# Optimization experiments

Measured on AMD Instinct MI355X. Metric: run time of the kernel, lower is better.

## Reference

```python
import jax, jax.numpy as jnp
import numpy as np

D_K = 64
SCALE = 1.0 / np.sqrt(D_K).astype(np.float32)
NEG_INF = -1e9


def setup_inputs() -> dict:
    key = jax.random.key(0)
    kq, kk, kv, km = jax.random.split(key, 4)
    B, H, S, D = 2, 16, 2048, D_K
    Q = jax.random.normal(kq, (B, H, S, D), dtype=jnp.float32)
    K = jax.random.normal(kk, (B, H, S, D), dtype=jnp.float32)
    V = jax.random.normal(kv, (B, H, S, D), dtype=jnp.float32)
    atten_mask = jax.random.randint(km, (B, H, S, S), 0, 2, dtype=jnp.int32)
    return {"Q": Q, "K": K, "V": V, "atten_mask": atten_mask}


def reference(Q, K, V, atten_mask):
    # scores: [B, H, Sq, Sk]
    scores = jnp.einsum("bhqd,bhkd->bhqk", Q, K) * SCALE
    scores = jnp.where(atten_mask.astype(bool), NEG_INF, scores)
    weights = jax.nn.softmax(scores, axis=-1)
    context = jnp.einsum("bhqk,bhkd->bhqd", weights, V)
    return (context, weights)
```

## Files before the change

kernel.cpp:

```cpp
#include <hip/hip_runtime.h>


#define S_LEN 2048
#define D_HEAD 64
#define BM 32
#define BN 64
#define NKB (S_LEN / BN)
#define CTX_ELEMS (2 * 16 * 2048 * 64)

typedef __attribute__((ext_vector_type(4))) float f32x4;
typedef __attribute__((ext_vector_type(8))) __bf16 bf16x8;
typedef __attribute__((ext_vector_type(2))) __bf16 bf16x2;

__device__ __forceinline__ bf16x8 pack8(f32x4 a, f32x4 b, float sc) {
    bf16x8 r;
    r[0] = (__bf16)(a[0] * sc); r[1] = (__bf16)(a[1] * sc);
    r[2] = (__bf16)(a[2] * sc); r[3] = (__bf16)(a[3] * sc);
    r[4] = (__bf16)(b[0] * sc); r[5] = (__bf16)(b[1] * sc);
    r[6] = (__bf16)(b[2] * sc); r[7] = (__bf16)(b[3] * sc);
    return r;
}


__global__ __launch_bounds__(256) void attn_fwd(
    const float* __restrict__ Qg, const float* __restrict__ Kg,
    const float* __restrict__ Vg, const int* __restrict__ Mg,
    float* __restrict__ outg)
{
    __shared__ __align__(16) __bf16 Vt[2][64][72];
    __shared__ __align__(16) __bf16 Pb[2][32][72];
    __shared__ unsigned short bmap[32][128];
    __shared__ float redl[4][32];
    __shared__ float invl[32];

    const int tid  = threadIdx.x;
    const int wave = tid >> 6;
    const int lane = tid & 63;
    const int c    = lane & 15;
    const int quad = lane >> 4;

    const int bid  = blockIdx.x;
    const int bh   = bid >> 6;
    const int row0 = (bid & 63) * BM;

    const float* Qh = Qg + (size_t)bh * S_LEN * D_HEAD;
    const float* Kh = Kg + (size_t)bh * S_LEN * D_HEAD;
    const float* Vh = Vg + (size_t)bh * S_LEN * D_HEAD;
    const int*   Mh = Mg + ((size_t)bh * S_LEN + row0) * S_LEN;
    float* ctx  = outg + ((size_t)bh * S_LEN + row0) * D_HEAD;
    float* wout = outg + (size_t)CTX_ELEMS + ((size_t)bh * S_LEN + row0) * S_LEN;

    bf16x8 aQ[2][2];
    #pragma unroll
    for (int t = 0; t < 2; ++t)
      #pragma unroll
      for (int h = 0; h < 2; ++h) {
        const float* p = Qh + (size_t)(row0 + 16 * t + c) * D_HEAD + 32 * h + quad * 8;
        aQ[t][h] = pack8(*(const f32x4*)p, *(const f32x4*)(p + 4), 0.125f);
      }

    f32x4 accO[2];
    accO[0] = (f32x4){0.f, 0.f, 0.f, 0.f};
    accO[1] = (f32x4){0.f, 0.f, 0.f, 0.f};
    float lacc[2][4] = {{0.f,0.f,0.f,0.f},{0.f,0.f,0.f,0.f}};

    const int vk2 = (tid & 31) * 2;
    const int vd8 = (tid >> 5) * 8;

    int buf = 0;
    for (int kb = 0; kb < NKB; ++kb) {
        const int k0 = kb * BN;

        {
            const float* vp = Vh + (size_t)(k0 + vk2) * D_HEAD + vd8;
            f32x4 r0a = *(const f32x4*)vp;
            f32x4 r0b = *(const f32x4*)(vp + 4);
            f32x4 r1a = *(const f32x4*)(vp + D_HEAD);
            f32x4 r1b = *(const f32x4*)(vp + D_HEAD + 4);
            #pragma unroll
            for (int i = 0; i < 4; ++i) {
                bf16x2 p0; p0[0] = (__bf16)r0a[i]; p0[1] = (__bf16)r1a[i];
                *(bf16x2*)&Vt[buf][vd8 + i][vk2] = p0;
                bf16x2 p1; p1[0] = (__bf16)r0b[i]; p1[1] = (__bf16)r1b[i];
                *(bf16x2*)&Vt[buf][vd8 + 4 + i][vk2] = p1;
            }
        }

        bf16x8 bK[2];
        #pragma unroll
        for (int h = 0; h < 2; ++h) {
            const float* p = Kh + (size_t)(k0 + 16 * wave + c) * D_HEAD + 32 * h + quad * 8;
            bK[h] = pack8(*(const f32x4*)p, *(const f32x4*)(p + 4), 1.0f);
        }
        f32x4 scv[2];
        scv[0] = (f32x4){0.f,0.f,0.f,0.f};
        scv[1] = (f32x4){0.f,0.f,0.f,0.f};
        #pragma unroll
        for (int h = 0; h < 2; ++h) {
            scv[0] = __builtin_amdgcn_mfma_f32_16x16x32_bf16(aQ[0][h], bK[h], scv[0], 0, 0, 0);
            scv[1] = __builtin_amdgcn_mfma_f32_16x16x32_bf16(aQ[1][h], bK[h], scv[1], 0, 0, 0);
        }

        #pragma unroll
        for (int t = 0; t < 2; ++t)
          #pragma unroll
          for (int r = 0; r < 4; ++r) {
            const int lrow = 16 * t + 4 * quad + r;
            const int col  = k0 + 16 * wave + c;
            const int mv   = __builtin_nontemporal_load(Mh + (size_t)lrow * S_LEN + col);
            const unsigned long long bal = __ballot(mv != 0);
            const float pv = mv ? 0.f : __expf(scv[t][r]);
            lacc[t][r] += pv;
            Pb[buf][lrow][16 * wave + c] = (__bf16)pv;
            if (c == 0)
                bmap[lrow][4 * kb + wave] = (unsigned short)(bal >> (16 * quad));
          }
        __syncthreads();

        #pragma unroll
        for (int h = 0; h < 2; ++h) {
            bf16x8 bV  = *(const bf16x8*)&Vt[buf][16 * wave + c][32 * h + quad * 8];
            bf16x8 aP0 = *(const bf16x8*)&Pb[buf][c][32 * h + quad * 8];
            bf16x8 aP1 = *(const bf16x8*)&Pb[buf][16 + c][32 * h + quad * 8];
            accO[0] = __builtin_amdgcn_mfma_f32_16x16x32_bf16(aP0, bV, accO[0], 0, 0, 0);
            accO[1] = __builtin_amdgcn_mfma_f32_16x16x32_bf16(aP1, bV, accO[1], 0, 0, 0);
        }
        buf ^= 1;
    }

    #pragma unroll
    for (int t = 0; t < 2; ++t)
      #pragma unroll
      for (int r = 0; r < 4; ++r) {
        float v = lacc[t][r];
        v += __shfl_xor(v, 1);
        v += __shfl_xor(v, 2);
        v += __shfl_xor(v, 4);
        v += __shfl_xor(v, 8);
        lacc[t][r] = v;
      }
    if (c == 0) {
        #pragma unroll
        for (int t = 0; t < 2; ++t)
          #pragma unroll
          for (int r = 0; r < 4; ++r)
            redl[wave][16 * t + 4 * quad + r] = lacc[t][r];
    }
    __syncthreads();
    if (tid < 32) {
        float s = redl[0][tid] + redl[1][tid] + redl[2][tid] + redl[3][tid];
        invl[tid] = 1.0f / s;
    }
    __syncthreads();

    float inv[2][4];
    #pragma unroll
    for (int t = 0; t < 2; ++t)
      #pragma unroll
      for (int r = 0; r < 4; ++r)
        inv[t][r] = invl[16 * t + 4 * quad + r];

    #pragma unroll
    for (int t = 0; t < 2; ++t)
      #pragma unroll
      for (int r = 0; r < 4; ++r)
        ctx[(size_t)(16 * t + 4 * quad + r) * D_HEAD + 16 * wave + c] = accO[t][r] * inv[t][r];

    for (int kb = 0; kb < NKB; ++kb) {
        const int k0 = kb * BN;
        bf16x8 bK[2];
        #pragma unroll
        for (int h = 0; h < 2; ++h) {
            const float* p = Kh + (size_t)(k0 + 16 * wave + c) * D_HEAD + 32 * h + quad * 8;
            bK[h] = pack8(*(const f32x4*)p, *(const f32x4*)(p + 4), 1.0f);
        }
        f32x4 scv[2];
        scv[0] = (f32x4){0.f,0.f,0.f,0.f};
        scv[1] = (f32x4){0.f,0.f,0.f,0.f};
        #pragma unroll
        for (int h = 0; h < 2; ++h) {
            scv[0] = __builtin_amdgcn_mfma_f32_16x16x32_bf16(aQ[0][h], bK[h], scv[0], 0, 0, 0);
            scv[1] = __builtin_amdgcn_mfma_f32_16x16x32_bf16(aQ[1][h], bK[h], scv[1], 0, 0, 0);
        }
        #pragma unroll
        for (int t = 0; t < 2; ++t)
          #pragma unroll
          for (int r = 0; r < 4; ++r) {
            const int lrow = 16 * t + 4 * quad + r;
            const unsigned bits = bmap[lrow][4 * kb + wave];
            const float pv = ((bits >> c) & 1u) ? 0.f : __expf(scv[t][r]) * inv[t][r];
            __builtin_nontemporal_store(pv, wout + (size_t)lrow * S_LEN + k0 + 16 * wave + c);
          }
    }
}

extern "C" void kernel_launch(void* const* d_in, const int* in_sizes, int n_in,
                              void* d_out, int out_size, void* d_ws, size_t ws_size,
                              hipStream_t stream) {
    const float* Q = (const float*)d_in[0];
    const float* K = (const float*)d_in[1];
    const float* V = (const float*)d_in[2];
    const int*   M = (const int*)d_in[3];
    float* out = (float*)d_out;
    dim3 grid(2048);
    dim3 block(256);
    attn_fwd<<<grid, block, 0, stream>>>(Q, K, V, M, out);
}
```

Baseline: 1.383 ms.

## Software-prefetch next K/V/mask tiles into registers in both attention passes

```diff
diff --git a/kernel.cpp b/kernel.cpp
--- a/kernel.cpp
+++ b/kernel.cpp
@@ -17,12 +17,24 @@
     r[0] = (__bf16)(a[0] * sc); r[1] = (__bf16)(a[1] * sc);
     r[2] = (__bf16)(a[2] * sc); r[3] = (__bf16)(a[3] * sc);
     r[4] = (__bf16)(b[0] * sc); r[5] = (__bf16)(b[1] * sc);
+    r[6] = (__bf16)(b[2] * sc); r[7] = (__bf16)(b[7 - 7] * sc);
     r[6] = (__bf16)(b[2] * sc); r[7] = (__bf16)(b[3] * sc);
     return r;
 }
 
-
-__global__ __launch_bounds__(256) void attn_fwd(
+#define MFMA16(a, b, c) __builtin_amdgcn_mfma_f32_16x16x32_bf16(a, b, c, 0, 0, 0)
+
+struct PF1 {
+    f32x4 v[4];
+    f32x4 k[4];
+    int   m[8];
+};
+struct PF2 {
+    f32x4 k[4];
+};
+
+
+__global__ __launch_bounds__(256, 4) void attn_fwd(
     const float* __restrict__ Qg, const float* __restrict__ Kg,
     const float* __restrict__ Vg, const int* __restrict__ Mg,
     float* __restrict__ outg)
@@ -67,65 +79,90 @@
     const int vk2 = (tid & 31) * 2;
     const int vd8 = (tid >> 5) * 8;
 
+#define ISSUE_V(P, KN) {                                                      \
+    const float* vp_ = Vh + (size_t)((KN) * BN + vk2) * D_HEAD + vd8;         \
+    (P).v[0] = *(const f32x4*)vp_;                                            \
+    (P).v[1] = *(const f32x4*)(vp_ + 4);                                      \
+    (P).v[2] = *(const f32x4*)(vp_ + D_HEAD);                                 \
+    (P).v[3] = *(const f32x4*)(vp_ + D_HEAD + 4); }
+
+#define ISSUE_K(P, KN) {                                                      \
+    const float* kp_ = Kh + (size_t)((KN) * BN + 16 * wave + c) * D_HEAD + quad * 8; \
+    (P).k[0] = *(const f32x4*)kp_;                                            \
+    (P).k[1] = *(const f32x4*)(kp_ + 4);                                      \
+    (P).k[2] = *(const f32x4*)(kp_ + 32);                                     \
+    (P).k[3] = *(const f32x4*)(kp_ + 36); }
+
+#define ISSUE_M(P, KN) {                                                      \
+    const int* mp_ = Mh + (KN) * BN + 16 * wave + c;                          \
+    _Pragma("unroll")                                                         \
+    for (int t_ = 0; t_ < 2; ++t_)                                            \
+      _Pragma("unroll")                                                       \
+      for (int r_ = 0; r_ < 4; ++r_)                                          \
+        (P).m[4 * t_ + r_] =                                                  \
+            __builtin_nontemporal_load(mp_ + (size_t)(16 * t_ + 4 * quad + r_) * S_LEN); }
+
+#define LDS_BARRIER() {                                                       \
+    asm volatile("s_waitcnt lgkmcnt(0)" ::: "memory");                        \
+    __builtin_amdgcn_s_barrier(); }
+
+#define P1BODY(KB, CUR, NXT) {                                                \
+    const int kn_ = ((KB) + 1 < NKB) ? (KB) + 1 : (KB);                       \
+        \
+    _Pragma("unroll")                                                         \
+    for (int i_ = 0; i_ < 4; ++i_) {                                          \
+        bf16x2 p0_; p0_[0] = (__bf16)CUR.v[0][i_]; p0_[1] = (__bf16)CUR.v[2][i_]; \
+        *(bf16x2*)&Vt[buf][vd8 + i_][vk2] = p0_;                              \
+        bf16x2 p1_; p1_[0] = (__bf16)CUR.v[1][i_]; p1_[1] = (__bf16)CUR.v[3][i_]; \
+        *(bf16x2*)&Vt[buf][vd8 + 4 + i_][vk2] = p1_;                          \
+    }                                                                         \
+    ISSUE_V(NXT, kn_);                                                        \
+                     \
+    bf16x8 bK0_ = pack8(CUR.k[0], CUR.k[1], 1.0f);                            \
+    bf16x8 bK1_ = pack8(CUR.k[2], CUR.k[3], 1.0f);                            \
+    ISSUE_K(NXT, kn_);                                                        \
+    f32x4 sc0_ = (f32x4){0.f, 0.f, 0.f, 0.f};                                 \
+    f32x4 sc1_ = (f32x4){0.f, 0.f, 0.f, 0.f};                                 \
+    sc0_ = MFMA16(aQ[0][0], bK0_, sc0_);                                      \
+    sc1_ = MFMA16(aQ[1][0], bK0_, sc1_);                                      \
+    sc0_ = MFMA16(aQ[0][1], bK1_, sc0_);                                      \
+    sc1_ = MFMA16(aQ[1][1], bK1_, sc1_);                                      \
+     \
+    _Pragma("unroll")                                                         \
+    for (int t_ = 0; t_ < 2; ++t_)                                            \
+      _Pragma("unroll")                                                       \
+      for (int r_ = 0; r_ < 4; ++r_) {                                        \
+        const int lrow_ = 16 * t_ + 4 * quad + r_;                            \
+        const int mv_   = CUR.m[4 * t_ + r_];                                 \
+        const unsigned long long bal_ = __ballot(mv_ != 0);                   \
+        const float sv_ = (t_ == 0) ? sc0_[r_] : sc1_[r_];                    \
+        const float pv_ = mv_ ? 0.f : __expf(sv_);                            \
+        lacc[t_][r_] += pv_;                                                  \
+        Pb[buf][lrow_][16 * wave + c] = (__bf16)pv_;                          \
+        if (c == 0)                                                           \
+            bmap[lrow_][4 * (KB) + wave] = (unsigned short)(bal_ >> (16 * quad)); \
+      }                                                                       \
+    ISSUE_M(NXT, kn_);                                                        \
+    LDS_BARRIER();                                                            \
+            \
+    _Pragma("unroll")                                                         \
+    for (int h_ = 0; h_ < 2; ++h_) {                                          \
+        bf16x8 bV_  = *(const bf16x8*)&Vt[buf][16 * wave + c][32 * h_ + quad * 8]; \
+        bf16x8 aP0_ = *(const bf16x8*)&Pb[buf][c][32 * h_ + quad * 8];        \
+        bf16x8 aP1_ = *(const bf16x8*)&Pb[buf][16 + c][32 * h_ + quad * 8];   \
+        accO[0] = MFMA16(aP0_, bV_, accO[0]);                                 \
+        accO[1] = MFMA16(aP1_, bV_, accO[1]);                                 \
+    }                                                                         \
+    buf ^= 1; }
+
     int buf = 0;
-    for (int kb = 0; kb < NKB; ++kb) {
-        const int k0 = kb * BN;
-
-        {
-            const float* vp = Vh + (size_t)(k0 + vk2) * D_HEAD + vd8;
-            f32x4 r0a = *(const f32x4*)vp;
-            f32x4 r0b = *(const f32x4*)(vp + 4);
-            f32x4 r1a = *(const f32x4*)(vp + D_HEAD);
-            f32x4 r1b = *(const f32x4*)(vp + D_HEAD + 4);
-            #pragma unroll
-            for (int i = 0; i < 4; ++i) {
-                bf16x2 p0; p0[0] = (__bf16)r0a[i]; p0[1] = (__bf16)r1a[i];
-                *(bf16x2*)&Vt[buf][vd8 + i][vk2] = p0;
-                bf16x2 p1; p1[0] = (__bf16)r0b[i]; p1[1] = (__bf16)r1b[i];
-                *(bf16x2*)&Vt[buf][vd8 + 4 + i][vk2] = p1;
-            }
-        }
-
-        bf16x8 bK[2];
-        #pragma unroll
-        for (int h = 0; h < 2; ++h) {
-            const float* p = Kh + (size_t)(k0 + 16 * wave + c) * D_HEAD + 32 * h + quad * 8;
-            bK[h] = pack8(*(const f32x4*)p, *(const f32x4*)(p + 4), 1.0f);
-        }
-        f32x4 scv[2];
-        scv[0] = (f32x4){0.f,0.f,0.f,0.f};
-        scv[1] = (f32x4){0.f,0.f,0.f,0.f};
-        #pragma unroll
-        for (int h = 0; h < 2; ++h) {
-            scv[0] = __builtin_amdgcn_mfma_f32_16x16x32_bf16(aQ[0][h], bK[h], scv[0], 0, 0, 0);
-            scv[1] = __builtin_amdgcn_mfma_f32_16x16x32_bf16(aQ[1][h], bK[h], scv[1], 0, 0, 0);
-        }
-
-        #pragma unroll
-        for (int t = 0; t < 2; ++t)
-          #pragma unroll
-          for (int r = 0; r < 4; ++r) {
-            const int lrow = 16 * t + 4 * quad + r;
-            const int col  = k0 + 16 * wave + c;
-            const int mv   = __builtin_nontemporal_load(Mh + (size_t)lrow * S_LEN + col);
-            const unsigned long long bal = __ballot(mv != 0);
-            const float pv = mv ? 0.f : __expf(scv[t][r]);
-            lacc[t][r] += pv;
-            Pb[buf][lrow][16 * wave + c] = (__bf16)pv;
-            if (c == 0)
-                bmap[lrow][4 * kb + wave] = (unsigned short)(bal >> (16 * quad));
-          }
-        __syncthreads();
-
-        #pragma unroll
-        for (int h = 0; h < 2; ++h) {
-            bf16x8 bV  = *(const bf16x8*)&Vt[buf][16 * wave + c][32 * h + quad * 8];
-            bf16x8 aP0 = *(const bf16x8*)&Pb[buf][c][32 * h + quad * 8];
-            bf16x8 aP1 = *(const bf16x8*)&Pb[buf][16 + c][32 * h + quad * 8];
-            accO[0] = __builtin_amdgcn_mfma_f32_16x16x32_bf16(aP0, bV, accO[0], 0, 0, 0);
-            accO[1] = __builtin_amdgcn_mfma_f32_16x16x32_bf16(aP1, bV, accO[1], 0, 0, 0);
-        }
-        buf ^= 1;
+    PF1 pf0, pf1;
+    ISSUE_V(pf0, 0);
+    ISSUE_K(pf0, 0);
+    ISSUE_M(pf0, 0);
+    for (int kb = 0; kb < NKB; kb += 2) {
+        P1BODY(kb,     pf0, pf1);
+        P1BODY(kb + 1, pf1, pf0);
     }
 
     #pragma unroll
@@ -166,31 +203,34 @@
       for (int r = 0; r < 4; ++r)
         ctx[(size_t)(16 * t + 4 * quad + r) * D_HEAD + 16 * wave + c] = accO[t][r] * inv[t][r];
 
-    for (int kb = 0; kb < NKB; ++kb) {
-        const int k0 = kb * BN;
-        bf16x8 bK[2];
-        #pragma unroll
-        for (int h = 0; h < 2; ++h) {
-            const float* p = Kh + (size_t)(k0 + 16 * wave + c) * D_HEAD + 32 * h + quad * 8;
-            bK[h] = pack8(*(const f32x4*)p, *(const f32x4*)(p + 4), 1.0f);
-        }
-        f32x4 scv[2];
-        scv[0] = (f32x4){0.f,0.f,0.f,0.f};
-        scv[1] = (f32x4){0.f,0.f,0.f,0.f};
-        #pragma unroll
-        for (int h = 0; h < 2; ++h) {
-            scv[0] = __builtin_amdgcn_mfma_f32_16x16x32_bf16(aQ[0][h], bK[h], scv[0], 0, 0, 0);
-            scv[1] = __builtin_amdgcn_mfma_f32_16x16x32_bf16(aQ[1][h], bK[h], scv[1], 0, 0, 0);
-        }
-        #pragma unroll
-        for (int t = 0; t < 2; ++t)
-          #pragma unroll
-          for (int r = 0; r < 4; ++r) {
-            const int lrow = 16 * t + 4 * quad + r;
-            const unsigned bits = bmap[lrow][4 * kb + wave];
-            const float pv = ((bits >> c) & 1u) ? 0.f : __expf(scv[t][r]) * inv[t][r];
-            __builtin_nontemporal_store(pv, wout + (size_t)lrow * S_LEN + k0 + 16 * wave + c);
-          }
+#define P2BODY(KB, CUR, NXT) {                                                \
+    const int kn_ = ((KB) + 1 < NKB) ? (KB) + 1 : (KB);                       \
+    ISSUE_K(NXT, kn_);                                                        \
+    bf16x8 bK0_ = pack8(CUR.k[0], CUR.k[1], 1.0f);                            \
+    bf16x8 bK1_ = pack8(CUR.k[2], CUR.k[3], 1.0f);                            \
+    f32x4 sc0_ = (f32x4){0.f, 0.f, 0.f, 0.f};                                 \
+    f32x4 sc1_ = (f32x4){0.f, 0.f, 0.f, 0.f};                                 \
+    sc0_ = MFMA16(aQ[0][0], bK0_, sc0_);                                      \
+    sc1_ = MFMA16(aQ[1][0], bK0_, sc1_);                                      \
+    sc0_ = MFMA16(aQ[0][1], bK1_, sc0_);                                      \
+    sc1_ = MFMA16(aQ[1][1], bK1_, sc1_);                                      \
+    const int k0_ = (KB) * BN;                                                \
+    _Pragma("unroll")                                                         \
+    for (int t_ = 0; t_ < 2; ++t_)                                            \
+      _Pragma("unroll")                                                       \
+      for (int r_ = 0; r_ < 4; ++r_) {                                        \
+        const int lrow_ = 16 * t_ + 4 * quad + r_;                            \
+        const unsigned bits_ = bmap[lrow_][4 * (KB) + wave];                  \
+        const float sv_ = (t_ == 0) ? sc0_[r_] : sc1_[r_];                    \
+        const float pv_ = ((bits_ >> c) & 1u) ? 0.f : __expf(sv_) * inv[t_][r_]; \
+        __builtin_nontemporal_store(pv_, wout + (size_t)lrow_ * S_LEN + k0_ + 16 * wave + c); \
+      } }
+
+    PF2 qf0, qf1;
+    ISSUE_K(qf0, 0);
+    for (int kb = 0; kb < NKB; kb += 2) {
+        P2BODY(kb,     qf0, qf1);
+        P2BODY(kb + 1, qf1, qf0);
     }
 }
 
```

Measured after the change: 1.282 ms. 7.3% less time.

## Keep mask bits in registers, single-buffer LDS, swizzle blocks, raise occupancy

Applied to the files above, without the earlier changes.

```diff
diff --git a/kernel.cpp b/kernel.cpp
--- a/kernel.cpp
+++ b/kernel.cpp
@@ -21,15 +21,20 @@
     return r;
 }
 
-
-__global__ __launch_bounds__(256) void attn_fwd(
+#define MFMA16(a, b, c) __builtin_amdgcn_mfma_f32_16x16x32_bf16(a, b, c, 0, 0, 0)
+
+#define LDS_BARRIER() {                                                       \
+    asm volatile("s_waitcnt lgkmcnt(0)" ::: "memory");                        \
+    __builtin_amdgcn_s_barrier(); }
+
+
+__global__ __launch_bounds__(256, 8) void attn_fwd(
     const float* __restrict__ Qg, const float* __restrict__ Kg,
     const float* __restrict__ Vg, const int* __restrict__ Mg,
     float* __restrict__ outg)
 {
-    __shared__ __align__(16) __bf16 Vt[2][64][72];
-    __shared__ __align__(16) __bf16 Pb[2][32][72];
-    __shared__ unsigned short bmap[32][128];
+    __shared__ __align__(16) __bf16 Vt[64][72];
+    __shared__ __align__(16) __bf16 Pb[32][72];
     __shared__ float redl[4][32];
     __shared__ float invl[32];
 
@@ -39,7 +44,7 @@
     const int c    = lane & 15;
     const int quad = lane >> 4;
 
-    const int bid  = blockIdx.x;
+    const int bid  = (blockIdx.x & 7) * (2048 / 8) + (blockIdx.x >> 3);
     const int bh   = bid >> 6;
     const int row0 = (bid & 63) * BM;
 
@@ -63,11 +68,11 @@
     accO[0] = (f32x4){0.f, 0.f, 0.f, 0.f};
     accO[1] = (f32x4){0.f, 0.f, 0.f, 0.f};
     float lacc[2][4] = {{0.f,0.f,0.f,0.f},{0.f,0.f,0.f,0.f}};
+    unsigned mreg[8] = {0u,0u,0u,0u,0u,0u,0u,0u};
 
     const int vk2 = (tid & 31) * 2;
     const int vd8 = (tid >> 5) * 8;
 
-    int buf = 0;
     for (int kb = 0; kb < NKB; ++kb) {
         const int k0 = kb * BN;
 
@@ -80,9 +85,9 @@
             #pragma unroll
             for (int i = 0; i < 4; ++i) {
                 bf16x2 p0; p0[0] = (__bf16)r0a[i]; p0[1] = (__bf16)r1a[i];
-                *(bf16x2*)&Vt[buf][vd8 + i][vk2] = p0;
+                *(bf16x2*)&Vt[vd8 + i][vk2] = p0;
                 bf16x2 p1; p1[0] = (__bf16)r0b[i]; p1[1] = (__bf16)r1b[i];
-                *(bf16x2*)&Vt[buf][vd8 + 4 + i][vk2] = p1;
+                *(bf16x2*)&Vt[vd8 + 4 + i][vk2] = p1;
             }
         }
 
@@ -97,35 +102,33 @@
         scv[1] = (f32x4){0.f,0.f,0.f,0.f};
         #pragma unroll
         for (int h = 0; h < 2; ++h) {
-            scv[0] = __builtin_amdgcn_mfma_f32_16x16x32_bf16(aQ[0][h], bK[h], scv[0], 0, 0, 0);
-            scv[1] = __builtin_amdgcn_mfma_f32_16x16x32_bf16(aQ[1][h], bK[h], scv[1], 0, 0, 0);
-        }
-
+            scv[0] = MFMA16(aQ[0][h], bK[h], scv[0]);
+            scv[1] = MFMA16(aQ[1][h], bK[h], scv[1]);
+        }
+
+        const int* mp = Mh + k0 + 16 * wave + c;
         #pragma unroll
         for (int t = 0; t < 2; ++t)
           #pragma unroll
           for (int r = 0; r < 4; ++r) {
             const int lrow = 16 * t + 4 * quad + r;
-            const int col  = k0 + 16 * wave + c;
-            const int mv   = __builtin_nontemporal_load(Mh + (size_t)lrow * S_LEN + col);
-            const unsigned long long bal = __ballot(mv != 0);
+            const int mv   = __builtin_nontemporal_load(mp + (size_t)lrow * S_LEN);
             const float pv = mv ? 0.f : __expf(scv[t][r]);
             lacc[t][r] += pv;
-            Pb[buf][lrow][16 * wave + c] = (__bf16)pv;
-            if (c == 0)
-                bmap[lrow][4 * kb + wave] = (unsigned short)(bal >> (16 * quad));
+            Pb[lrow][16 * wave + c] = (__bf16)pv;
+            mreg[4 * t + r] |= (mv ? 1u : 0u) << kb;
           }
-        __syncthreads();
-
-        #pragma unroll
-        for (int h = 0; h < 2; ++h) {
-            bf16x8 bV  = *(const bf16x8*)&Vt[buf][16 * wave + c][32 * h + quad * 8];
-            bf16x8 aP0 = *(const bf16x8*)&Pb[buf][c][32 * h + quad * 8];
-            bf16x8 aP1 = *(const bf16x8*)&Pb[buf][16 + c][32 * h + quad * 8];
-            accO[0] = __builtin_amdgcn_mfma_f32_16x16x32_bf16(aP0, bV, accO[0], 0, 0, 0);
-            accO[1] = __builtin_amdgcn_mfma_f32_16x16x32_bf16(aP1, bV, accO[1], 0, 0, 0);
-        }
-        buf ^= 1;
+        LDS_BARRIER();
+
+        #pragma unroll
+        for (int h = 0; h < 2; ++h) {
+            bf16x8 bV  = *(const bf16x8*)&Vt[16 * wave + c][32 * h + quad * 8];
+            bf16x8 aP0 = *(const bf16x8*)&Pb[c][32 * h + quad * 8];
+            bf16x8 aP1 = *(const bf16x8*)&Pb[16 + c][32 * h + quad * 8];
+            accO[0] = MFMA16(aP0, bV, accO[0]);
+            accO[1] = MFMA16(aP1, bV, accO[1]);
+        }
+        LDS_BARRIER();
     }
 
     #pragma unroll
@@ -179,16 +182,16 @@
         scv[1] = (f32x4){0.f,0.f,0.f,0.f};
         #pragma unroll
         for (int h = 0; h < 2; ++h) {
-            scv[0] = __builtin_amdgcn_mfma_f32_16x16x32_bf16(aQ[0][h], bK[h], scv[0], 0, 0, 0);
-            scv[1] = __builtin_amdgcn_mfma_f32_16x16x32_bf16(aQ[1][h], bK[h], scv[1], 0, 0, 0);
+            scv[0] = MFMA16(aQ[0][h], bK[h], scv[0]);
+            scv[1] = MFMA16(aQ[1][h], bK[h], scv[1]);
         }
         #pragma unroll
         for (int t = 0; t < 2; ++t)
           #pragma unroll
           for (int r = 0; r < 4; ++r) {
             const int lrow = 16 * t + 4 * quad + r;
-            const unsigned bits = bmap[lrow][4 * kb + wave];
-            const float pv = ((bits >> c) & 1u) ? 0.f : __expf(scv[t][r]) * inv[t][r];
+            const unsigned bit = (mreg[4 * t + r] >> kb) & 1u;
+            const float pv = bit ? 0.f : __expf(scv[t][r]) * inv[t][r];
             __builtin_nontemporal_store(pv, wout + (size_t)lrow * S_LEN + k0 + 16 * wave + c);
           }
     }
```

Result: no change. 1.376 ms (-0.5%).
